# Kernel tuning notes

Hardware: AMD Instinct MI355X
Metric: run time of the kernel (lower is better)

## Reference

```python
import jax, jax.numpy as jnp
import numpy as np

B, G, C, Hmlp, R = 4, 2048, 384, 1536, 96
NH = 6          # attention heads
V = 6           # number of 2D views (len(out_transform_2d))
NC = 1024       # number of clusters for segment_csr
GX = GY = 32    # grid shape per view
SCALE_FACTOR = 0.5  # args.scale_factor
COEF_PRO = 0.5      # args.coef_pro
EPS_LN = 1e-5
EPS_BN = 1e-5


def _forward(x, center1, norm1_g, norm1_b, qkv_w, proj_w, proj_b, norm2_g, norm2_b,
             fc1_w, fc1_b, fc2_w, fc2_b, ada1_w, ada1_b, ada2_w, ada2_b,
             bn3_g, bn3_b, bn3_m, bn3_v, bn2_g, bn2_b, bn2_m, bn2_v,
             norm3_g, norm3_b, a1_qkv_w, a1_proj_w, a1_proj_b,
             mask, idx_ptr, sorted_cluster_indices, cluster, flat_grid_index,
             grid_shape_x, grid_shape_y):
    B_, G1, C_ = x.shape
    hd = C_ // NH

    def ln(t, g, b):
        mu = t.mean(-1, keepdims=True)
        var = ((t - mu) ** 2).mean(-1, keepdims=True)
        return (t - mu) * jax.lax.rsqrt(var + EPS_LN) * g + b

    def bn_gelu(t, g, b, m, v):  # BatchNorm1d (eval) + GELU
        t = (t - m) * jax.lax.rsqrt(v + EPS_BN) * g + b
        return jax.nn.gelu(t, approximate=False)

    # ---- multi-head self-attention sublayer ----
    h = ln(x, norm1_g, norm1_b)
    qkv = (h @ qkv_w).reshape(B_, G1, 3, NH, hd).transpose(2, 0, 3, 1, 4)
    q, k, v = qkv[0], qkv[1], qkv[2]
    attn = jax.nn.softmax(jnp.einsum('bhqd,bhkd->bhqk', q, k) * hd ** -0.5, axis=-1)
    o = jnp.einsum('bhqk,bhkd->bhqd', attn, v).transpose(0, 2, 1, 3).reshape(B_, G1, C_)
    x = x + o @ proj_w + proj_b

    # ---- MLP + adapter sublayer ----
    h2 = ln(x, norm2_g, norm2_b)
    ffn = jax.nn.gelu(h2 @ fc1_w + fc1_b, approximate=False) @ fc2_w + fc2_b
    a = ffn @ ada1_w + ada1_b
    a = a * jax.nn.sigmoid(1.702 * a)      # QuickGELU
    ada = a @ ada2_w + ada2_b
    x = x + ffn + SCALE_FACTOR * ada

    cls_x = x[:, :1]
    pts = x[:, 1:]
    Gp = G1 - 1
    N = B_ * Gp

    # ---- 3D branch: segment_csr max/mean over clusters, gather back ----
    feat = pts.reshape(N, C_)
    fs = feat[sorted_cluster_indices]
    seg = cluster[sorted_cluster_indices]          # sorted segment ids (CSR order)
    nc = idx_ptr.shape[0] - 1
    cnt = jax.ops.segment_sum(jnp.ones((N,), feat.dtype), seg, nc)
    fsum = jax.ops.segment_sum(fs, seg, nc)
    fmax = jax.ops.segment_max(fs, seg, nc)
    fmax = jnp.where(cnt[:, None] > 0, fmax, 0.0)
    fmean = fsum / jnp.maximum(cnt, 1.0)[:, None]
    x3d = bn_gelu(fmax + fmean, bn3_g, bn3_b, bn3_m, bn3_v)[cluster].reshape(pts.shape)

    # ---- per-view 2D branch: masked attn + scatter_max/mean over grid cells ----
    dim_size = center1.shape[0] * grid_shape_x * grid_shape_y
    nviews = center1.shape[1]
    views = []
    for i in range(nviews):
        fx = pts.reshape(N, C_)
        h3 = ln(fx, norm3_g[i], norm3_b[i]).reshape(B_, Gp, C_)
        qkv1 = (h3 @ a1_qkv_w[i]).reshape(B_, Gp, 3, C_).transpose(2, 0, 1, 3)
        q1, k1, v1 = qkv1[0], qkv1[1], qkv1[2]
        s = jnp.einsum('bqd,bkd->bqk', q1, k1) * C_ ** -0.5
        s = jnp.where(mask[i][None], s, jnp.finfo(s.dtype).min)
        o1 = jnp.einsum('bqk,bkd->bqd', jax.nn.softmax(s, axis=-1), v1) @ a1_proj_w[i] + a1_proj_b[i]
        fx = o1.reshape(N, C_) + fx
        gi = flat_grid_index[i]
        gc = jax.ops.segment_sum(jnp.ones((N,), fx.dtype), gi, dim_size)
        gs = jax.ops.segment_sum(fx, gi, dim_size)
        gm = jax.ops.segment_max(fx, gi, dim_size)
        gm = jnp.where(gc[:, None] > 0, gm, 0.0)
        cell = bn_gelu(gs / jnp.maximum(gc, 1.0)[:, None] + gm,
                       bn2_g[i], bn2_b[i], bn2_m[i], bn2_v[i])
        views.append(cell[gi].reshape(pts.shape))

    # ---- cosine-similarity weighted fusion across views ----
    x_sup = jnp.stack(views, 0)                     # [V,B,G,C]
    dot = jnp.sum(x_sup * x3d[None], -1)
    nrm = jnp.linalg.norm(x_sup, axis=-1) * jnp.linalg.norm(x3d, axis=-1)[None]
    sims = (dot / jnp.maximum(nrm, 1e-8) + 1.0) / 2.0
    sims = sims / sims.sum(0, keepdims=True)
    x_sup_w = jnp.sum(x_sup * sims[..., None], 0)
    pts = pts + COEF_PRO * x_sup_w
    return jnp.concatenate([cls_x, pts], axis=1)


def setup_inputs() -> dict:
    rng = np.random.default_rng(0)
    key = jax.random.key(0)
    N = B * G
    # consistent cluster structure: every cluster non-empty
    cluster = np.concatenate([np.arange(NC), rng.integers(0, NC, N - NC)]).astype(np.int32)
    rng.shuffle(cluster)
    sorted_idx = np.argsort(cluster, kind='stable').astype(np.int32)
    counts = np.bincount(cluster, minlength=NC)
    idx_ptr = np.concatenate([[0], np.cumsum(counts)]).astype(np.int32)
    flat_grid_index = rng.integers(0, B * GX * GY, (V, N)).astype(np.int32)
    mask = (rng.random((V, G, G)) < 0.25) | np.eye(G, dtype=bool)[None]
    ks = jax.random.split(key, 16)
    f32 = jnp.float32
    def w(k, shape, s=0.02):
        return jax.random.normal(k, shape, f32) * s
    return {
        'x': jax.random.normal(ks[0], (B, G + 1, C), f32),
        'center1': jax.random.normal(ks[1], (B, V, G, 3), f32),
        'norm1_g': jnp.ones((C,), f32), 'norm1_b': jnp.zeros((C,), f32),
        'qkv_w': w(ks[2], (C, 3 * C)), 'proj_w': w(ks[3], (C, C)), 'proj_b': jnp.zeros((C,), f32),
        'norm2_g': jnp.ones((C,), f32), 'norm2_b': jnp.zeros((C,), f32),
        'fc1_w': w(ks[4], (C, Hmlp)), 'fc1_b': jnp.zeros((Hmlp,), f32),
        'fc2_w': w(ks[5], (Hmlp, C)), 'fc2_b': jnp.zeros((C,), f32),
        'ada1_w': w(ks[6], (C, R)), 'ada1_b': jnp.zeros((R,), f32),
        'ada2_w': w(ks[7], (R, C)), 'ada2_b': jnp.zeros((C,), f32),
        'bn3_g': jnp.ones((C,), f32), 'bn3_b': jnp.zeros((C,), f32),
        'bn3_m': w(ks[8], (C,), 0.1), 'bn3_v': jnp.ones((C,), f32) + jax.random.uniform(ks[9], (C,), f32) * 0.5,
        'bn2_g': jnp.ones((V, C), f32), 'bn2_b': jnp.zeros((V, C), f32),
        'bn2_m': w(ks[10], (V, C), 0.1), 'bn2_v': jnp.ones((V, C), f32) + jax.random.uniform(ks[11], (V, C), f32) * 0.5,
        'norm3_g': jnp.ones((V, C), f32), 'norm3_b': jnp.zeros((V, C), f32),
        'a1_qkv_w': w(ks[12], (V, C, 3 * C)), 'a1_proj_w': w(ks[13], (V, C, C)), 'a1_proj_b': jnp.zeros((V, C), f32),
        'mask': jnp.asarray(mask),
        'idx_ptr': jnp.asarray(idx_ptr),
        'sorted_cluster_indices': jnp.asarray(sorted_idx),
        'cluster': jnp.asarray(cluster),
        'flat_grid_index': jnp.asarray(flat_grid_index),
        'grid_shape_x': GX,
        'grid_shape_y': GY,
    }


def reference(x, center1, norm1_g, norm1_b, qkv_w, proj_w, proj_b, norm2_g, norm2_b,
              fc1_w, fc1_b, fc2_w, fc2_b, ada1_w, ada1_b, ada2_w, ada2_b,
              bn3_g, bn3_b, bn3_m, bn3_v, bn2_g, bn2_b, bn2_m, bn2_v,
              norm3_g, norm3_b, a1_qkv_w, a1_proj_w, a1_proj_b,
              mask, idx_ptr, sorted_cluster_indices, cluster, flat_grid_index,
              grid_shape_x, grid_shape_y):
    return _forward(x, center1, norm1_g, norm1_b, qkv_w, proj_w, proj_b, norm2_g, norm2_b,
                    fc1_w, fc1_b, fc2_w, fc2_b, ada1_w, ada1_b, ada2_w, ada2_b,
                    bn3_g, bn3_b, bn3_m, bn3_v, bn2_g, bn2_b, bn2_m, bn2_v,
                    norm3_g, norm3_b, a1_qkv_w, a1_proj_w, a1_proj_b,
                    mask, idx_ptr, sorted_cluster_indices, cluster, flat_grid_index,
                    grid_shape_x, grid_shape_y)
```

## Files before the change

### kernel.cpp

```cpp
#include <hip/hip_runtime.h>
#include <math.h>

typedef short bf16x8 __attribute__((ext_vector_type(8)));
typedef float f32x4 __attribute__((ext_vector_type(4)));

#define GLL16(g, l) \
  __builtin_amdgcn_global_load_lds((__attribute__((address_space(1))) const unsigned int*)(g), \
                                   (__attribute__((address_space(3))) unsigned int*)(l), 16, 0, 0)

__device__ __forceinline__ float wsum(float v){
  #pragma unroll
  for (int o=32;o;o>>=1) v += __shfl_xor(v,o);
  return v;
}
__device__ __forceinline__ float geluf(float x){
  return 0.5f*x*(1.0f+erff(x*0.7071067811865475f));
}
__device__ __forceinline__ short fbf(float f){
  unsigned u = __float_as_uint(f);
  unsigned r = (u + 0x7fffu + ((u>>16)&1u)) >> 16;
  return (short)r;
}
__device__ __forceinline__ float bff(short s){
  return __uint_as_float(((unsigned)(unsigned short)s)<<16);
}
__device__ __forceinline__ unsigned fkey(float f){
  unsigned b=__float_as_uint(f);
  return (b&0x80000000u)? ~b : (b|0x80000000u);
}
__device__ __forceinline__ float fdec(unsigned k){
  unsigned b=(k&0x80000000u)? (k&0x7fffffffu) : ~k;
  return __uint_as_float(b);
}

__global__ void detect_mask_kernel(const int* __restrict__ m, long long n, int* flag){
  long long i = (long long)blockIdx.x*256 + threadIdx.x;
  bool bad = (i<n) && (m[i]!=0 && m[i]!=1);
  if (__any(bad)) { if ((threadIdx.x&63)==0) atomicOr(flag,1); }
}
__global__ void mask_byte_kernel(const void* __restrict__ m, unsigned char* __restrict__ mb,
                                 long long n4, const int* __restrict__ flag){
  long long i = (long long)blockIdx.x*256 + threadIdx.x;
  if (i>=n4) return;
  int mode = *flag;
  uchar4 o;
  if (mode){ o = ((const uchar4*)m)[i]; o.x=o.x!=0; o.y=o.y!=0; o.z=o.z!=0; o.w=o.w!=0; }
  else { int4 v = ((const int4*)m)[i];
         o.x=(unsigned char)(v.x!=0); o.y=(unsigned char)(v.y!=0);
         o.z=(unsigned char)(v.z!=0); o.w=(unsigned char)(v.w!=0); }
  ((uchar4*)mb)[i]=o;
}

__device__ __forceinline__ float epi(float v, const float* bias, int col, int act){
  if (bias) v += bias[col];
  if (act==1) v = geluf(v);
  else if (act==2) v = v*(1.f/(1.f+__expf(-1.702f*v)));
  return v;
}

#define XBM 128
#define XBN 128
#define XBK 32
__global__ __launch_bounds__(256)
void gemm_bf16_big(const short* __restrict__ A, int lda, long long sA,
                   const short* __restrict__ B, int ldb, long long sB,
                   const float* __restrict__ bias, long long sBias,
                   const float* __restrict__ res, int ldr, long long sR,
                   void* __restrict__ out, int ldo, long long sO, int outbf16,
                   int M, int N, int K, int act, int KS)
{
  __shared__ short As[XBM*XBK];
  __shared__ short Bs[XBN*XBK];
  int zz = blockIdx.z;
  int z = zz / KS, ks = zz - z*KS;
  A += (long long)z*sA; B += (long long)z*sB;
  if (res) res += (long long)z*sR;
  if (bias) bias += (long long)z*sBias;
  float* outF = (float*)out + (long long)z*sO;
  short* outH = (short*)out + (long long)z*sO;

  int tid = threadIdx.x;
  int rowBase = blockIdx.y*XBM;
  int colBase = blockIdx.x*XBN;

  int Kc = ((K + KS*XBK - 1)/(KS*XBK))*XBK;
  int kbeg = ks*Kc;
  int kend = min(K, kbeg+Kc);
  if (kbeg >= kend) return;

  int w = tid>>6;
  int lane = tid&63;
  int lm = lane&15, quad = lane>>4;
  int waveM = w>>1, waveN = w&1;

  int arow0 = min(rowBase + w*32 + lm,      M-1);
  int arow1 = min(rowBase + w*32 + 16 + lm, M-1);
  int brow0 = min(colBase + w*32 + lm,      N-1);
  int brow1 = min(colBase + w*32 + 16 + lm, N-1);
  const short* Ag0 = A + (long long)arow0*lda + quad*8;
  const short* Ag1 = A + (long long)arow1*lda + quad*8;
  const short* Bg0 = B + (long long)brow0*ldb + quad*8;
  const short* Bg1 = B + (long long)brow1*ldb + quad*8;
  short* Al0 = &As[(w*2+0)*512];
  short* Al1 = &As[(w*2+1)*512];
  short* Bl0 = &Bs[(w*2+0)*512];
  short* Bl1 = &Bs[(w*2+1)*512];

  f32x4 acc[4][4] = {};

  for (int k0=kbeg; k0<kend; k0+=XBK){
    GLL16(Ag0 + k0, Al0);
    GLL16(Ag1 + k0, Al1);
    GLL16(Bg0 + k0, Bl0);
    GLL16(Bg1 + k0, Bl1);
    __syncthreads();
    bf16x8 af[4], bfr[4];
    #pragma unroll
    for (int tm=0;tm<4;tm++) af[tm]  = *(bf16x8*)&As[(waveM*4+tm)*512 + quad*128 + lm*8];
    #pragma unroll
    for (int tn=0;tn<4;tn++) bfr[tn] = *(bf16x8*)&Bs[(waveN*4+tn)*512 + quad*128 + lm*8];
    #pragma unroll
    for (int tm=0;tm<4;tm++)
      #pragma unroll
      for (int tn=0;tn<4;tn++)
        acc[tm][tn] = __builtin_amdgcn_mfma_f32_16x16x32_bf16(af[tm], bfr[tn], acc[tm][tn], 0,0,0);
    __syncthreads();
  }

  #pragma unroll
  for (int tm=0;tm<4;tm++){
    #pragma unroll
    for (int tn=0;tn<4;tn++){
      int col = colBase + waveN*64 + tn*16 + lm;
      if (col>=N) continue;
      #pragma unroll
      for (int reg=0;reg<4;reg++){
        int row = rowBase + waveM*64 + tm*16 + quad*4 + reg;
        if (row>=M) continue;
        float v = acc[tm][tn][reg];
        if (KS>1){ atomicAdd(&outF[(long long)row*ldo+col], v); continue; }
        v = epi(v, bias, col, act);
        if (res) v += res[(long long)row*ldr+col];
        if (outbf16) outH[(long long)row*ldo+col] = fbf(v);
        else         outF[(long long)row*ldo+col] = v;
      }
    }
  }
}

__global__ __launch_bounds__(256)
void gemm_bf16_s(const short* __restrict__ A, int lda, long long sA,
                 const short* __restrict__ B, int ldb, long long sB,
                 const float* __restrict__ bias, long long sBias,
                 const float* __restrict__ res, int ldr, long long sR,
                 void* __restrict__ out, int ldo, long long sO, int outbf16,
                 int M, int N, int K, int act)
{
  __shared__ short As[64*32];
  __shared__ short Bs[64*32];
  int z = blockIdx.z;
  A += (long long)z*sA; B += (long long)z*sB;
  if (res) res += (long long)z*sR;
  if (bias) bias += (long long)z*sBias;
  float* outF = (float*)out + (long long)z*sO;
  short* outH = (short*)out + (long long)z*sO;

  int tid = threadIdx.x;
  int rowBase = blockIdx.y*64;
  int colBase = blockIdx.x*64;

  int w = tid>>6;
  int lane = tid&63;
  int lm = lane&15, quad = lane>>4;
  int wm = w>>1, wn = w&1;

  int arow = min(rowBase + w*16 + lm, M-1);
  int brow = min(colBase + w*16 + lm, N-1);
  const short* Ag = A + (long long)arow*lda + quad*8;
  const short* Bg = B + (long long)brow*ldb + quad*8;
  short* Al = &As[w*512];
  short* Bl = &Bs[w*512];

  f32x4 acc[2][2] = {};

  for (int k0=0; k0<K; k0+=32){
    GLL16(Ag + k0, Al);
    GLL16(Bg + k0, Bl);
    __syncthreads();
    bf16x8 af[2], bfr[2];
    #pragma unroll
    for (int tm=0;tm<2;tm++) af[tm]  = *(bf16x8*)&As[(wm*2+tm)*512 + quad*128 + lm*8];
    #pragma unroll
    for (int tn=0;tn<2;tn++) bfr[tn] = *(bf16x8*)&Bs[(wn*2+tn)*512 + quad*128 + lm*8];
    #pragma unroll
    for (int tm=0;tm<2;tm++)
      #pragma unroll
      for (int tn=0;tn<2;tn++)
        acc[tm][tn] = __builtin_amdgcn_mfma_f32_16x16x32_bf16(af[tm], bfr[tn], acc[tm][tn], 0,0,0);
    __syncthreads();
  }

  #pragma unroll
  for (int tm=0;tm<2;tm++){
    #pragma unroll
    for (int tn=0;tn<2;tn++){
      int col = colBase + wn*32 + tn*16 + lm;
      if (col>=N) continue;
      #pragma unroll
      for (int reg=0;reg<4;reg++){
        int row = rowBase + wm*32 + tm*16 + quad*4 + reg;
        if (row>=M) continue;
        float v = epi(acc[tm][tn][reg], bias, col, act);
        if (res) v += res[(long long)row*ldr+col];
        if (outbf16==2){
          int bb = row>>11;
          outH[((long long)bb*384 + col)*2048 + (row&2047)] = fbf(v);
        }
        else if (outbf16) outH[(long long)row*ldo+col] = fbf(v);
        else              outF[(long long)row*ldo+col] = v;
      }
    }
  }
}

__global__ __launch_bounds__(256,2)
void flash_view(const short* __restrict__ QK6, const short* __restrict__ Vt6,
                const unsigned char* __restrict__ maskb, short* __restrict__ O6)
{
  __shared__ char lds[58112];
  const float scale = 0.05103103630798288f;
  int id = blockIdx.x;
  int xcd = id & 7;
  int j = id >> 3;
  int vb = xcd*3 + (j>>5);
  int qt = j & 31;
  int v = vb >> 2, b = vb & 3;
  int tid=threadIdx.x, w=tid>>6, lane=tid&63, lm=lane&15, quad=lane>>4;

  const short* Qp = QK6 + ((long long)v*8192 + b*2048 + qt*64)*768;
  const short* Kp = QK6 + ((long long)v*8192 + b*2048)*768 + 384;
  const short* Vp = Vt6 + (long long)(v*4+b)*384*2048;
  const unsigned char* Mp = maskb + (long long)v*2048*2048 + (long long)qt*64*2048;
  short* Op = O6 + ((long long)v*8192 + b*2048 + qt*64)*384;

  short* P = (short*)(lds + 49152);
  float* alphaL = (float*)(lds + 57856);

  bf16x8 af[12];
  #pragma unroll
  for (int c=0;c<12;c++)
    af[c] = *(const bf16x8*)(Qp + (long long)(w*16+lm)*768 + c*32 + quad*8);

  float m_i[4], l_i[4];
  #pragma unroll
  for (int r=0;r<4;r++){ m_i[r]=-3.0e38f; l_i[r]=0.f; }
  f32x4 Oacc[4][6] = {};

  #pragma unroll
  for (int c=0;c<12;c++)
    GLL16(Kp + (long long)(w*16 + lm)*768 + c*32 + quad*8, (short*)(lds + w*12288 + c*1024));

  for (int kt=0; kt<32; kt++){
    __syncthreads();
    unsigned char mreg[4][4];
    #pragma unroll
    for (int ct=0;ct<4;ct++)
      #pragma unroll
      for (int r=0;r<4;r++)
        mreg[ct][r] = Mp[(long long)(w*16+quad*4+r)*2048 + kt*64 + ct*16 + lm];
    f32x4 S[4];
    #pragma unroll
    for (int i=0;i<4;i++) S[i] = (f32x4){0.f,0.f,0.f,0.f};
    #pragma unroll
    for (int kc=0;kc<12;kc++){
      #pragma unroll
      for (int ct=0;ct<4;ct++){
        bf16x8 bf = *(bf16x8*)(lds + ct*12288 + kc*1024 + quad*256 + lm*16);
        S[ct] = __builtin_amdgcn_mfma_f32_16x16x32_bf16(af[kc], bf, S[ct], 0,0,0);
      }
    }
    #pragma unroll
    for (int ct=0;ct<4;ct++){
      #pragma unroll
      for (int r=0;r<4;r++)
        S[ct][r] = mreg[ct][r] ? S[ct][r]*scale : -3.0e38f;
    }
    float alpha[4], mnew[4];
    #pragma unroll
    for (int r=0;r<4;r++){
      float rm = S[0][r];
      #pragma unroll
      for (int ct=1;ct<4;ct++) rm = fmaxf(rm, S[ct][r]);
      #pragma unroll
      for (int o=1;o<16;o<<=1) rm = fmaxf(rm, __shfl_xor(rm, o));
      mnew[r] = fmaxf(m_i[r], rm);
      alpha[r] = __expf(m_i[r]-mnew[r]);
      m_i[r] = mnew[r];
    }
    float rs[4] = {0.f,0.f,0.f,0.f};
    #pragma unroll
    for (int ct=0;ct<4;ct++){
      #pragma unroll
      for (int r=0;r<4;r++){
        float sv = S[ct][r];
        float p = (sv > -1.0e37f) ? __expf(sv - mnew[r]) : 0.f;
        rs[r] += p;
        P[(w*16+quad*4+r)*68 + ct*16 + lm] = fbf(p);
      }
    }
    #pragma unroll
    for (int r=0;r<4;r++){
      #pragma unroll
      for (int o=1;o<16;o<<=1) rs[r] += __shfl_xor(rs[r], o);
      l_i[r] = l_i[r]*alpha[r] + rs[r];
    }
    if (lm==0){
      #pragma unroll
      for (int r=0;r<4;r++) alphaL[w*16+quad*4+r] = alpha[r];
    }
    bf16x8 Vreg[6][2];
    #pragma unroll
    for (int jj=0;jj<6;jj++)
      #pragma unroll
      for (int kk=0;kk<2;kk++)
        Vreg[jj][kk] = *(const bf16x8*)(Vp + (long long)((w*6+jj)*16+lm)*2048 + kt*64 + kk*32 + quad*8);
    __syncthreads();
    if (kt < 31){
      #pragma unroll
      for (int c=0;c<12;c++)
        GLL16(Kp + (long long)((kt+1)*64 + w*16 + lm)*768 + c*32 + quad*8,
              (short*)(lds + w*12288 + c*1024));
    }
    f32x4 am[4];
    #pragma unroll
    for (int m=0;m<4;m++) am[m] = *(f32x4*)&alphaL[m*16 + quad*4];
    #pragma unroll
    for (int m=0;m<4;m++)
      #pragma unroll
      for (int tn=0;tn<6;tn++)
        Oacc[m][tn] *= am[m];
    #pragma unroll
    for (int kk=0;kk<2;kk++){
      bf16x8 ap[4];
      #pragma unroll
      for (int m=0;m<4;m++) ap[m] = *(bf16x8*)&P[(m*16+lm)*68 + kk*32 + quad*8];
      #pragma unroll
      for (int tn=0;tn<6;tn++){
        #pragma unroll
        for (int m=0;m<4;m++)
          Oacc[m][tn] = __builtin_amdgcn_mfma_f32_16x16x32_bf16(ap[m], Vreg[tn][kk], Oacc[m][tn], 0,0,0);
      }
    }
  }

  __syncthreads();
  if (lm==0){
    #pragma unroll
    for (int r=0;r<4;r++) alphaL[w*16+quad*4+r] = l_i[r];
  }
  __syncthreads();
  f32x4 lv[4];
  #pragma unroll
  for (int m=0;m<4;m++) lv[m] = *(f32x4*)&alphaL[m*16 + quad*4];
  #pragma unroll
  for (int m=0;m<4;m++){
    #pragma unroll
    for (int tn=0;tn<6;tn++){
      #pragma unroll
      for (int reg=0;reg<4;reg++){
        Op[(long long)(m*16+quad*4+reg)*384 + (w*6+tn)*16 + lm] = fbf(Oacc[m][tn][reg] / lv[m][reg]);
      }
    }
  }
}

__global__ __launch_bounds__(256,4)
void flash_inner(const short* __restrict__ QKV, const short* __restrict__ Vt,
                 short* __restrict__ O)
{
  __shared__ char lds[17152];
  int id = blockIdx.x;
  int xcd = id & 7;
  int j = id >> 3;
  int bh = xcd*3 + j/33;
  int qt = j%33;
  int b=bh/6, h=bh-b*6;
  int tid=threadIdx.x, w=tid>>6, lane=tid&63, lm=lane&15, quad=lane>>4;

  const short* Qb = QKV + (long long)b*2049*1152 + h*64;
  const short* Kb = Qb + 384;
  const short* Vtp = Vt + (long long)bh*64*2112;
  short* Op = O + ((long long)b*2049 + qt*64)*384 + h*64;

  short* P = (short*)(lds + 8192);
  float* alphaL = (float*)(lds + 16896);

  int qr = min(qt*64 + w*16 + lm, 2048);
  bf16x8 af[2];
  #pragma unroll
  for (int c=0;c<2;c++)
    af[c] = *(const bf16x8*)(Qb + (long long)qr*1152 + c*32 + quad*8);

  float m_i[4], l_i[4];
  #pragma unroll
  for (int r=0;r<4;r++){ m_i[r]=-3.0e38f; l_i[r]=0.f; }
  f32x4 Oacc[4] = {};

  {
    int kr0 = min(w*16 + lm, 2048);
    #pragma unroll
    for (int c=0;c<2;c++)
      GLL16(Kb + (long long)kr0*1152 + c*32 + quad*8, (short*)(lds + w*2048 + c*1024));
  }

  for (int kt=0; kt<33; kt++){
    __syncthreads();
    f32x4 S[4];
    #pragma unroll
    for (int i=0;i<4;i++) S[i] = (f32x4){0.f,0.f,0.f,0.f};
    #pragma unroll
    for (int kc=0;kc<2;kc++){
      #pragma unroll
      for (int ct=0;ct<4;ct++){
        bf16x8 bf = *(bf16x8*)(lds + ct*2048 + kc*1024 + quad*256 + lm*16);
        S[ct] = __builtin_amdgcn_mfma_f32_16x16x32_bf16(af[kc], bf, S[ct], 0,0,0);
      }
    }
    #pragma unroll
    for (int ct=0;ct<4;ct++){
      int scol = kt*64 + ct*16 + lm;
      bool ok = scol <= 2048;
      #pragma unroll
      for (int r=0;r<4;r++) S[ct][r] = ok ? S[ct][r]*0.125f : -3.0e38f;
    }
    float alpha[4], mnew[4];
    #pragma unroll
    for (int r=0;r<4;r++){
      float rm = S[0][r];
      #pragma unroll
      for (int ct=1;ct<4;ct++) rm = fmaxf(rm, S[ct][r]);
      #pragma unroll
      for (int o=1;o<16;o<<=1) rm = fmaxf(rm, __shfl_xor(rm, o));
      mnew[r] = fmaxf(m_i[r], rm);
      alpha[r] = __expf(m_i[r]-mnew[r]);
      m_i[r] = mnew[r];
    }
    float rs[4] = {0.f,0.f,0.f,0.f};
    #pragma unroll
    for (int ct=0;ct<4;ct++){
      #pragma unroll
      for (int r=0;r<4;r++){
        float sv = S[ct][r];
        float p = (sv > -1.0e37f) ? __expf(sv - mnew[r]) : 0.f;
        rs[r] += p;
        P[(w*16+quad*4+r)*68 + ct*16 + lm] = fbf(p);
      }
    }
    #pragma unroll
    for (int r=0;r<4;r++){
      #pragma unroll
      for (int o=1;o<16;o<<=1) rs[r] += __shfl_xor(rs[r], o);
      l_i[r] = l_i[r]*alpha[r] + rs[r];
    }
    if (lm==0){
      #pragma unroll
      for (int r=0;r<4;r++) alphaL[w*16+quad*4+r] = alpha[r];
    }
    bf16x8 Vreg[2];
    #pragma unroll
    for (int kk=0;kk<2;kk++)
      Vreg[kk] = *(const bf16x8*)(Vtp + (long long)(w*16+lm)*2112 + kt*64 + kk*32 + quad*8);
    __syncthreads();
    if (kt < 32){
      int krn = min((kt+1)*64 + w*16 + lm, 2048);
      #pragma unroll
      for (int c=0;c<2;c++)
        GLL16(Kb + (long long)krn*1152 + c*32 + quad*8, (short*)(lds + w*2048 + c*1024));
    }
    f32x4 am[4];
    #pragma unroll
    for (int m=0;m<4;m++) am[m] = *(f32x4*)&alphaL[m*16 + quad*4];
    #pragma unroll
    for (int m=0;m<4;m++) Oacc[m] *= am[m];
    #pragma unroll
    for (int kk=0;kk<2;kk++){
      bf16x8 ap[4];
      #pragma unroll
      for (int m=0;m<4;m++) ap[m] = *(bf16x8*)&P[(m*16+lm)*68 + kk*32 + quad*8];
      #pragma unroll
      for (int m=0;m<4;m++)
        Oacc[m] = __builtin_amdgcn_mfma_f32_16x16x32_bf16(ap[m], Vreg[kk], Oacc[m], 0,0,0);
    }
  }

  __syncthreads();
  if (lm==0){
    #pragma unroll
    for (int r=0;r<4;r++) alphaL[w*16+quad*4+r] = l_i[r];
  }
  __syncthreads();
  f32x4 lv[4];
  #pragma unroll
  for (int m=0;m<4;m++) lv[m] = *(f32x4*)&alphaL[m*16 + quad*4];
  #pragma unroll
  for (int m=0;m<4;m++){
    #pragma unroll
    for (int reg=0;reg<4;reg++){
      int row = qt*64 + m*16 + quad*4 + reg;
      if (row < 2049)
        Op[(long long)(m*16+quad*4+reg)*384 + w*16 + lm] = fbf(Oacc[m][reg] / lv[m][reg]);
    }
  }
}

__global__ __launch_bounds__(128)
void ln_bf16_kernel(const float* __restrict__ in, const float* __restrict__ g,
                    const float* __restrict__ bt, short* __restrict__ out)
{
  long long row = blockIdx.x;
  const float* p = in + row*384;
  int tid = threadIdx.x;
  float v0=p[tid], v1=p[tid+128], v2=p[tid+256];
  float s = v0+v1+v2;
  float ss = v0*v0+v1*v1+v2*v2;
  __shared__ float r1[2], r2[2];
  s = wsum(s); ss = wsum(ss);
  int wid=tid>>6, lane=tid&63;
  if (lane==0){ r1[wid]=s; r2[wid]=ss; }
  __syncthreads();
  float mean=(r1[0]+r1[1])*(1.f/384.f);
  float var =(r2[0]+r2[1])*(1.f/384.f)-mean*mean;
  float rstd=rsqrtf(var+1e-5f);
  short* o = out + row*384;
  o[tid]     = fbf((v0-mean)*rstd*g[tid]+bt[tid]);
  o[tid+128] = fbf((v1-mean)*rstd*g[tid+128]+bt[tid+128]);
  o[tid+256] = fbf((v2-mean)*rstd*g[tid+256]+bt[tid+256]);
}

__global__ __launch_bounds__(128)
void ln6_kernel(const float* __restrict__ in, const float* __restrict__ g6,
                const float* __restrict__ b6, short* __restrict__ out6)
{
  long long row = blockIdx.x;
  const float* p = in + row*384;
  int tid = threadIdx.x;
  float v0=p[tid], v1=p[tid+128], v2=p[tid+256];
  float s = v0+v1+v2;
  float ss = v0*v0+v1*v1+v2*v2;
  __shared__ float r1[2], r2[2];
  s = wsum(s); ss = wsum(ss);
  int wid=tid>>6, lane=tid&63;
  if (lane==0){ r1[wid]=s; r2[wid]=ss; }
  __syncthreads();
  float mean=(r1[0]+r1[1])*(1.f/384.f);
  float var =(r2[0]+r2[1])*(1.f/384.f)-mean*mean;
  float rstd=rsqrtf(var+1e-5f);
  float n0=(v0-mean)*rstd, n1=(v1-mean)*rstd, n2=(v2-mean)*rstd;
  #pragma unroll
  for (int i=0;i<6;i++){
    const float* g = g6 + i*384;
    const float* bt = b6 + i*384;
    short* o = out6 + (long long)i*8192*384 + row*384;
    o[tid]     = fbf(n0*g[tid]+bt[tid]);
    o[tid+128] = fbf(n1*g[tid+128]+bt[tid+128]);
    o[tid+256] = fbf(n2*g[tid+256]+bt[tid+256]);
  }
}

__global__ void cvt_kernel(const float* __restrict__ in, short* __restrict__ out, long long n4){
  long long i = (long long)blockIdx.x*256 + threadIdx.x;
  if (i<n4){
    float4 f = ((const float4*)in)[i];
    short4 s;
    s.x=fbf(f.x); s.y=fbf(f.y); s.z=fbf(f.z); s.w=fbf(f.w);
    ((short4*)out)[i]=s;
  }
}

__global__ __launch_bounds__(256)
void tconv_kernel(const float* __restrict__ in, int ldin, long long sIn, long long sIn2, int zmod,
                  int R, int C, short* __restrict__ out, int ldout, long long sOut)
{
  __shared__ float tile[32][33];
  int z = blockIdx.z;
  const float* ip = in + (long long)(z/zmod)*sIn + (long long)(z%zmod)*sIn2;
  short* op = out + (long long)z*sOut;
  int r0 = blockIdx.x*32;
  int c0 = blockIdx.y*32;
  int tx = threadIdx.x&31, ty = threadIdx.x>>5;
  #pragma unroll
  for (int i=0;i<4;i++){
    int r = r0 + ty + i*8, c = c0 + tx;
    tile[ty+i*8][tx] = (r<R && c<C) ? ip[(long long)r*ldin + c] : 0.f;
  }
  __syncthreads();
  #pragma unroll
  for (int i=0;i<4;i++){
    int oc = c0 + ty + i*8;
    int orr = r0 + tx;
    if (oc<C && orr<ldout) op[(long long)oc*ldout + orr] = fbf(tile[tx][ty+i*8]);
  }
}

__global__ __launch_bounds__(256)
void tconv16_kernel(const short* __restrict__ in, int ldin, long long sIn, long long sIn2, int zmod,
                    int R, int C, short* __restrict__ out, int ldout, long long sOut)
{
  __shared__ short tile[32][34];
  int z = blockIdx.z;
  const short* ip = in + (long long)(z/zmod)*sIn + (long long)(z%zmod)*sIn2;
  short* op = out + (long long)z*sOut;
  int r0 = blockIdx.x*32;
  int c0 = blockIdx.y*32;
  int tx = threadIdx.x&31, ty = threadIdx.x>>5;
  #pragma unroll
  for (int i=0;i<4;i++){
    int r = r0 + ty + i*8, c = c0 + tx;
    tile[ty+i*8][tx] = (r<R && c<C) ? ip[(long long)r*ldin + c] : (short)0;
  }
  __syncthreads();
  #pragma unroll
  for (int i=0;i<4;i++){
    int oc = c0 + ty + i*8;
    int orr = r0 + tx;
    if (oc<C && orr<ldout) op[(long long)oc*ldout + orr] = tile[tx][ty+i*8];
  }
}

__global__ void ew_x2_kernel(float* x1, const float* ffn, const float* ada, long long n){
  long long i=(long long)blockIdx.x*256+threadIdx.x;
  if (i<n) x1[i] = x1[i] + ffn[i] + 0.5f*ada[i];
}
__global__ void copy_pts_kernel(const float* __restrict__ x2, float* __restrict__ pts){
  long long i=(long long)blockIdx.x*256+threadIdx.x;
  if (i < 8192ll*384){
    long long b = i/(2048ll*384);
    long long rem = i%(2048ll*384);
    pts[i] = x2[(b*2049+1)*384 + rem];
  }
}
__global__ void copy_cls_kernel(const float* __restrict__ x2, float* __restrict__ out){
  int i = blockIdx.x*256+threadIdx.x;
  if (i < 4*384){
    int b=i/384, c=i%384;
    out[(long long)b*2049*384 + c] = x2[(long long)b*2049*384 + c];
  }
}

__global__ __launch_bounds__(128)
void scatter_seg_kernel(const float* __restrict__ feat, const int* __restrict__ seg,
                        float* __restrict__ fsum, unsigned* __restrict__ fmax,
                        float* __restrict__ cnt,
                        long long zFeat, long long zSeg, long long zSum, long long zCnt)
{
  int n = blockIdx.x, z = blockIdx.y;
  feat += (long long)z*zFeat; seg += (long long)z*zSeg;
  fsum += (long long)z*zSum; fmax += (long long)z*zSum; cnt += (long long)z*zCnt;
  int s = seg[n];
  const float* p = feat + (long long)n*384;
  int tid = threadIdx.x;
  #pragma unroll
  for (int k=0;k<3;k++){
    int c = tid + k*128;
    float v = p[c];
    atomicAdd(&fsum[(long long)s*384+c], v);
    atomicMax(&fmax[(long long)s*384+c], fkey(v));
  }
  if (tid==0) atomicAdd(&cnt[s], 1.0f);
}

__global__ __launch_bounds__(128)
void cell_kernel(const float* __restrict__ fsum, const unsigned* __restrict__ fmax,
                 const float* __restrict__ cnt,
                 const float* __restrict__ g, const float* __restrict__ bb,
                 const float* __restrict__ m, const float* __restrict__ v,
                 float* __restrict__ out, long long zSum, long long zCnt, long long zP)
{
  int s = blockIdx.x, z = blockIdx.y;
  fsum += (long long)z*zSum; fmax += (long long)z*zSum; cnt += (long long)z*zCnt;
  g += (long long)z*zP; bb += (long long)z*zP; m += (long long)z*zP; v += (long long)z*zP;
  out += (long long)z*zSum;
  float cn = cnt[s];
  float denom = fmaxf(cn, 1.f);
  int tid = threadIdx.x;
  #pragma unroll
  for (int k=0;k<3;k++){
    int c = tid + k*128;
    float mx = (cn>0.f) ? fdec(fmax[(long long)s*384+c]) : 0.f;
    float t = mx + fsum[(long long)s*384+c]/denom;
    t = (t - m[c])*rsqrtf(v[c]+1e-5f)*g[c] + bb[c];
    out[(long long)s*384+c] = geluf(t);
  }
}

__global__ __launch_bounds__(128)
void combine_kernel(const float* __restrict__ pts, const float* __restrict__ cell3,
                    const int* __restrict__ cluster, const float* __restrict__ cell2,
                    const int* __restrict__ gidx, float* __restrict__ out)
{
  int n = blockIdx.x;
  int tid = threadIdx.x;
  __shared__ float sdot[6], ssq[6], sw[6];
  __shared__ int soff[6];
  __shared__ float red[2][2];
  __shared__ float sn3;
  const float* x3 = cell3 + (long long)cluster[n]*384;
  int wid=tid>>6, lane=tid&63;
  float sq=0.f;
  for (int c=tid;c<384;c+=128){ float v=x3[c]; sq+=v*v; }
  sq = wsum(sq);
  if (lane==0) red[0][wid]=sq;
  __syncthreads();
  if (tid==0) sn3 = sqrtf(red[0][0]+red[0][1]);
  __syncthreads();
  for (int i=0;i<6;i++){
    int gi = gidx[(long long)i*8192 + n];
    if (tid==0) soff[i]=gi;
    const float* r = cell2 + ((long long)i*4096 + gi)*384;
    float d=0.f, s2=0.f;
    for (int c=tid;c<384;c+=128){ float a=r[c]; d+=a*x3[c]; s2+=a*a; }
    d = wsum(d); s2 = wsum(s2);
    if (lane==0){ red[0][wid]=d; red[1][wid]=s2; }
    __syncthreads();
    if (tid==0){ sdot[i]=red[0][0]+red[0][1]; ssq[i]=red[1][0]+red[1][1]; }
    __syncthreads();
  }
  if (tid==0){
    float ssumv=0.f; float sims[6];
    for (int i=0;i<6;i++){
      float nrm = sqrtf(ssq[i])*sn3;
      float s = (sdot[i]/fmaxf(nrm,1e-8f) + 1.f)*0.5f;
      sims[i]=s; ssumv+=s;
    }
    for (int i=0;i<6;i++) sw[i]=sims[i]/ssumv;
  }
  __syncthreads();
  int b = n>>11, gp = n&2047;
  float* o = out + ((long long)(b*2049 + 1 + gp))*384;
  for (int c=tid;c<384;c+=128){
    float acc=0.f;
    #pragma unroll
    for (int i=0;i<6;i++){
      const float* r = cell2 + ((long long)i*4096 + soff[i])*384;
      acc += sw[i]*r[c];
    }
    o[c] = pts[(long long)n*384+c] + 0.5f*acc;
  }
}

static inline void launch_gemm16b(hipStream_t s, const short* A,int lda,long long sA,
  const short* B,int ldb,long long sB, const float* bias, long long sBias,
  const float* res,int ldr,long long sR, void* out,int ldo,long long sO,int outbf16,
  int M,int N,int K,int act,int nz,int KS)
{
  dim3 g((N+XBN-1)/XBN,(M+XBM-1)/XBM,(unsigned)(nz*KS));
  hipLaunchKernelGGL(gemm_bf16_big,g,dim3(256),0,s,
    A,lda,sA,B,ldb,sB,bias,sBias,res,ldr,sR,out,ldo,sO,outbf16,M,N,K,act,KS);
}
static inline void launch_gemm16s(hipStream_t s, const short* A,int lda,long long sA,
  const short* B,int ldb,long long sB, const float* bias, long long sBias,
  const float* res,int ldr,long long sR, void* out,int ldo,long long sO,int outbf16,
  int M,int N,int K,int act,int nz)
{
  dim3 g((N+63)/64,(M+63)/64,(unsigned)nz);
  hipLaunchKernelGGL(gemm_bf16_s,g,dim3(256),0,s,
    A,lda,sA,B,ldb,sB,bias,sBias,res,ldr,sR,out,ldo,sO,outbf16,M,N,K,act);
}
static inline void launch_tconv(hipStream_t s, const float* in,int ldin,long long sIn,long long sIn2,int zmod,
  int R,int C, short* out,int ldout,long long sOut,int nz)
{
  dim3 g((ldout+31)/32,(C+31)/32,(unsigned)nz);
  hipLaunchKernelGGL(tconv_kernel,g,dim3(256),0,s, in,ldin,sIn,sIn2,zmod,R,C,out,ldout,sOut);
}
static inline void launch_tconv16(hipStream_t s, const short* in,int ldin,long long sIn,long long sIn2,int zmod,
  int R,int C, short* out,int ldout,long long sOut,int nz)
{
  dim3 g((ldout+31)/32,(C+31)/32,(unsigned)nz);
  hipLaunchKernelGGL(tconv16_kernel,g,dim3(256),0,s, in,ldin,sIn,sIn2,zmod,R,C,out,ldout,sOut);
}
static inline void launch_cvt(hipStream_t s, const float* in, short* out, long long n){
  long long n4 = n/4;
  hipLaunchKernelGGL(cvt_kernel,dim3((unsigned)((n4+255)/256)),dim3(256),0,s,in,out,n4);
}

extern "C" void kernel_launch(void* const* d_in, const int* in_sizes, int n_in,
                              void* d_out, int out_size, void* d_ws, size_t ws_size,
                              hipStream_t stream)
{
  const float* x       = (const float*)d_in[0];
  const float* norm1_g = (const float*)d_in[2];
  const float* norm1_b = (const float*)d_in[3];
  const float* qkv_w   = (const float*)d_in[4];
  const float* proj_w  = (const float*)d_in[5];
  const float* proj_b  = (const float*)d_in[6];
  const float* norm2_g = (const float*)d_in[7];
  const float* norm2_b = (const float*)d_in[8];
  const float* fc1_w   = (const float*)d_in[9];
  const float* fc1_b   = (const float*)d_in[10];
  const float* fc2_w   = (const float*)d_in[11];
  const float* fc2_b   = (const float*)d_in[12];
  const float* ada1_w  = (const float*)d_in[13];
  const float* ada1_b  = (const float*)d_in[14];
  const float* ada2_w  = (const float*)d_in[15];
  const float* ada2_b  = (const float*)d_in[16];
  const float* bn3_g   = (const float*)d_in[17];
  const float* bn3_b   = (const float*)d_in[18];
  const float* bn3_m   = (const float*)d_in[19];
  const float* bn3_v   = (const float*)d_in[20];
  const float* bn2_g   = (const float*)d_in[21];
  const float* bn2_b   = (const float*)d_in[22];
  const float* bn2_m   = (const float*)d_in[23];
  const float* bn2_v   = (const float*)d_in[24];
  const float* norm3_g = (const float*)d_in[25];
  const float* norm3_b = (const float*)d_in[26];
  const float* a1_qkv_w  = (const float*)d_in[27];
  const float* a1_proj_w = (const float*)d_in[28];
  const float* a1_proj_b = (const float*)d_in[29];
  const void*  maskp     = d_in[30];
  const int*   cluster   = (const int*)d_in[33];
  const int*   fgi       = (const int*)d_in[34];
  float* out = (float*)d_out;

  size_t off = 0;
  char* wsb = (char*)d_ws;
  auto alloc = [&](size_t bytes)->void*{
    void* p = wsb + off;
    off += (bytes + 255) & ~(size_t)255;
    return p;
  };
  short*    bufHh = (short*)alloc(8196ll*384*2);
  float*    ptsb  = (float*)alloc(8192ll*384*4);
  float*    cnt   = (float*)alloc(1024*4);
  float*    fsum  = (float*)alloc(1024ll*384*4);
  unsigned* fmaxe = (unsigned*)alloc(1024ll*384*4);
  float*    cell3 = (float*)alloc(1024ll*384*4);
  unsigned char* maskb = (unsigned char*)alloc(6ll*2048*2048);
  float*    gc6   = (float*)alloc(6ll*4096*4);
  short*    qkvT  = (short*)alloc(1152ll*384*2);
  short*    projT = (short*)alloc(384ll*384*2);
  short*    fc1T  = (short*)alloc(1536ll*384*2);
  short*    fc2T  = (short*)alloc(384ll*1536*2);
  short*    ada1T = (short*)alloc(96ll*384*2);
  short*    ada2T = (short*)alloc(384ll*96*2);
  short*    a1qkvT  = (short*)alloc(6ll*1152*384*2);
  short*    a1projT = (short*)alloc(6ll*384*384*2);
  int*      flag  = (int*)alloc(256);
  char* arena = (char*)alloc(188743680);
  char* A0 = arena;
  char* A1 = arena + 75497472;
  char* A2 = arena + 150994944;
  short* bufQh = (short*)(A0 + 0);
  float* bufO  = (float*)(A0 + 20971520);
  short* bufOh = (short*)(A0 + 35651584);
  short* bufAh = (short*)(A0 + 44040192);
  float* bufX  = (float*)(A0 + 46137344);
  float* bufAda= (float*)(A0 + 0);
  short* Vt_i  = (short*)(A1 + 0);
  short* bufTh = (short*)(A1 + 8388608);
  short* QK6   = (short*)(A0 + 0);
  short* Vt6   = (short*)(A1 + 0);
  short* O6    = (short*)(A2 + 0);
  short* bufHh6= (short*)(A2 + 0);
  float* bufT6 = (float*)(A0 + 0);
  float* gsum6 = (float*)(A1 + 0);
  unsigned* gmaxe6 = (unsigned*)(A1 + 37748736);
  float* cell2 = (float*)(A0 + 0);

  hipMemsetAsync(flag, 0, 4, stream);
  {
    long long nInt = 6ll*2048*2048/4;
    detect_mask_kernel<<<dim3((unsigned)((nInt+255)/256)),dim3(256),0,stream>>>((const int*)maskp, nInt, flag);
    mask_byte_kernel<<<dim3((unsigned)((nInt+255)/256)),dim3(256),0,stream>>>(maskp, maskb, nInt, flag);
  }

  launch_tconv(stream, qkv_w, 1152, 0,0,1, 384,1152, qkvT, 384, 0, 1);
  launch_tconv(stream, proj_w, 384, 0,0,1, 384,384,  projT, 384, 0, 1);
  launch_tconv(stream, fc1_w, 1536, 0,0,1, 384,1536, fc1T, 384, 0, 1);
  launch_tconv(stream, fc2_w, 384,  0,0,1, 1536,384, fc2T, 1536, 0, 1);
  launch_tconv(stream, ada1_w, 96,  0,0,1, 384,96,   ada1T, 384, 0, 1);
  launch_tconv(stream, ada2_w, 384, 0,0,1, 96,384,   ada2T, 96, 0, 1);
  launch_tconv(stream, a1_qkv_w, 1152, 384ll*1152,0,1, 384,1152, a1qkvT, 384, 1152ll*384, 6);
  launch_tconv(stream, a1_proj_w, 384, 384ll*384,0,1, 384,384,  a1projT, 384, 384ll*384, 6);

  ln_bf16_kernel<<<8196,128,0,stream>>>(x, norm1_g, norm1_b, bufHh);
  launch_gemm16b(stream, bufHh,384,0, qkvT,384,0, nullptr,0, nullptr,0,0,
                 bufQh,1152,0,1, 8196,1152,384, 0, 1,1);
  launch_tconv16(stream, bufQh + 768, 1152, 2049ll*1152, 64, 6, 2049, 64, Vt_i, 2112, 64ll*2112, 24);
  flash_inner<<<dim3(792),256,0,stream>>>(bufQh, Vt_i, bufOh);
  launch_gemm16s(stream, bufOh,384,0, projT,384,0, proj_b,0, x,384,0,
                 bufX,384,0,0, 8196,384,384, 0, 1);
  ln_bf16_kernel<<<8196,128,0,stream>>>(bufX, norm2_g, norm2_b, bufHh);
  launch_gemm16b(stream, bufHh,384,0, fc1T,384,0, fc1_b,0, nullptr,0,0,
                 bufTh,1536,0,1, 8196,1536,384, 1, 1,1);
  launch_gemm16s(stream, bufTh,1536,0, fc2T,1536,0, fc2_b,0, nullptr,0,0,
                 bufO,384,0,0, 8196,384,1536, 0, 1);
  launch_cvt(stream, bufO, bufOh, 8196ll*384);
  launch_gemm16s(stream, bufOh,384,0, ada1T,384,0, ada1_b,0, nullptr,0,0,
                 bufAh,96,0,1, 8196,96,384, 2, 1);
  launch_gemm16s(stream, bufAh,96,0, ada2T,96,0, ada2_b,0, nullptr,0,0,
                 bufAda,384,0,0, 8196,384,96, 0, 1);
  ew_x2_kernel<<<dim3((8196*384+255)/256),256,0,stream>>>(bufX, bufO, bufAda, 8196ll*384);
  copy_cls_kernel<<<6,256,0,stream>>>(bufX, out);
  copy_pts_kernel<<<dim3((8192*384+255)/256),256,0,stream>>>(bufX, ptsb);

  hipMemsetAsync(cnt, 0, 1024*4, stream);
  hipMemsetAsync(fsum, 0, 1024ll*384*4, stream);
  hipMemsetAsync(fmaxe, 0, 1024ll*384*4, stream);
  scatter_seg_kernel<<<dim3(8192,1),128,0,stream>>>(ptsb, cluster, fsum, fmaxe, cnt, 0,0,0,0);
  cell_kernel<<<dim3(1024,1),128,0,stream>>>(fsum, fmaxe, cnt, bn3_g,bn3_b,bn3_m,bn3_v, cell3, 0,0,0);

  ln6_kernel<<<8192,128,0,stream>>>(ptsb, norm3_g, norm3_b, bufHh6);
  launch_gemm16b(stream, bufHh6,384,8192ll*384, a1qkvT,384,1152ll*384,
                 nullptr,0, nullptr,0,0, QK6,768,8192ll*768,1, 8192,768,384, 0, 6,1);
  launch_gemm16s(stream, bufHh6,384,8192ll*384, a1qkvT + 768ll*384,384,1152ll*384,
                 nullptr,0, nullptr,0,0, Vt6,2048,4ll*384*2048,2, 8192,384,384, 0, 6);

  flash_view<<<dim3(768),256,0,stream>>>(QK6, Vt6, maskb, O6);

  launch_gemm16s(stream, O6,384,8192ll*384, a1projT,384,384ll*384,
                 a1_proj_b,384, ptsb,384,0,
                 bufT6,384,8192ll*384,0, 8192,384,384, 0, 6);
  hipMemsetAsync(gc6, 0, 6ll*4096*4, stream);
  hipMemsetAsync(gsum6, 0, 6ll*4096*384*4, stream);
  hipMemsetAsync(gmaxe6, 0, 6ll*4096*384*4, stream);
  scatter_seg_kernel<<<dim3(8192,6),128,0,stream>>>(bufT6, fgi, gsum6, gmaxe6, gc6,
      8192ll*384, 8192, 4096ll*384, 4096);
  cell_kernel<<<dim3(4096,6),128,0,stream>>>(gsum6, gmaxe6, gc6,
      bn2_g, bn2_b, bn2_m, bn2_v, cell2, 4096ll*384, 4096, 384);

  combine_kernel<<<8192,128,0,stream>>>(ptsb, cell3, cluster, cell2, fgi, out);
}
```

Measured before the change: 1.596 ms.

## Bit-pack attention mask, reschedule K loads, and raise MFMA wave priority

Replaces the byte-per-element mask with a 64-bit bitmask per row chunk, so each flash_view thread loads four 64-bit words instead of sixteen scattered bytes per tile. The K-tile global-to-LDS load moves from after the second barrier (prefetching the next tile) to the top of each iteration. s_setprio is raised around the MFMA blocks in both flash kernels. Removing the prefetch loses overlap of the K load with the PV MFMAs, which could offset the smaller mask traffic.

```diff
diff --git a/kernel.cpp b/kernel.cpp
--- a/kernel.cpp
+++ b/kernel.cpp
@@ -38,17 +38,33 @@
   bool bad = (i<n) && (m[i]!=0 && m[i]!=1);
   if (__any(bad)) { if ((threadIdx.x&63)==0) atomicOr(flag,1); }
 }
-__global__ void mask_byte_kernel(const void* __restrict__ m, unsigned char* __restrict__ mb,
-                                 long long n4, const int* __restrict__ flag){
+__global__ void mask_bits_kernel(const void* __restrict__ m, unsigned long long* __restrict__ mb,
+                                 long long nOut, const int* __restrict__ flag){
   long long i = (long long)blockIdx.x*256 + threadIdx.x;
-  if (i>=n4) return;
+  if (i>=nOut) return;
   int mode = *flag;
-  uchar4 o;
-  if (mode){ o = ((const uchar4*)m)[i]; o.x=o.x!=0; o.y=o.y!=0; o.z=o.z!=0; o.w=o.w!=0; }
-  else { int4 v = ((const int4*)m)[i];
-         o.x=(unsigned char)(v.x!=0); o.y=(unsigned char)(v.y!=0);
-         o.z=(unsigned char)(v.z!=0); o.w=(unsigned char)(v.w!=0); }
-  ((uchar4*)mb)[i]=o;
+  unsigned long long bits = 0;
+  if (mode){
+    const unsigned long long* p = (const unsigned long long*)((const unsigned char*)m + i*64);
+    #pragma unroll
+    for (int k=0;k<8;k++){
+      unsigned long long v = p[k];
+      #pragma unroll
+      for (int b=0;b<8;b++)
+        bits |= (unsigned long long)(((v>>(b*8))&0xffull)!=0) << (k*8+b);
+    }
+  } else {
+    const int4* p = (const int4*)((const int*)m + i*64);
+    #pragma unroll
+    for (int k=0;k<16;k++){
+      int4 v = p[k];
+      bits |= (unsigned long long)(v.x!=0) << (k*4+0);
+      bits |= (unsigned long long)(v.y!=0) << (k*4+1);
+      bits |= (unsigned long long)(v.z!=0) << (k*4+2);
+      bits |= (unsigned long long)(v.w!=0) << (k*4+3);
+    }
+  }
+  mb[i] = bits;
 }
 
 __device__ __forceinline__ float epi(float v, const float* bias, int col, int act){
@@ -225,7 +241,7 @@
 
 __global__ __launch_bounds__(256,2)
 void flash_view(const short* __restrict__ QK6, const short* __restrict__ Vt6,
-                const unsigned char* __restrict__ maskb, short* __restrict__ O6)
+                const unsigned long long* __restrict__ maskbits, short* __restrict__ O6)
 {
   __shared__ char lds[58112];
   const float scale = 0.05103103630798288f;
@@ -240,7 +256,7 @@
   const short* Qp = QK6 + ((long long)v*8192 + b*2048 + qt*64)*768;
   const short* Kp = QK6 + ((long long)v*8192 + b*2048)*768 + 384;
   const short* Vp = Vt6 + (long long)(v*4+b)*384*2048;
-  const unsigned char* Mp = maskb + (long long)v*2048*2048 + (long long)qt*64*2048;
+  const unsigned long long* Mb = maskbits + (long long)v*2048*32 + (long long)qt*64*32;
   short* Op = O6 + ((long long)v*8192 + b*2048 + qt*64)*384;
 
   short* P = (short*)(lds + 49152);
@@ -256,21 +272,19 @@
   for (int r=0;r<4;r++){ m_i[r]=-3.0e38f; l_i[r]=0.f; }
   f32x4 Oacc[4][6] = {};
 
-  #pragma unroll
-  for (int c=0;c<12;c++)
-    GLL16(Kp + (long long)(w*16 + lm)*768 + c*32 + quad*8, (short*)(lds + w*12288 + c*1024));
-
   for (int kt=0; kt<32; kt++){
+    #pragma unroll
+    for (int c=0;c<12;c++)
+      GLL16(Kp + (long long)(kt*64 + w*16 + lm)*768 + c*32 + quad*8, (short*)(lds + w*12288 + c*1024));
     __syncthreads();
-    unsigned char mreg[4][4];
-    #pragma unroll
-    for (int ct=0;ct<4;ct++)
-      #pragma unroll
-      for (int r=0;r<4;r++)
-        mreg[ct][r] = Mp[(long long)(w*16+quad*4+r)*2048 + kt*64 + ct*16 + lm];
+    unsigned long long mb[4];
+    #pragma unroll
+    for (int r=0;r<4;r++)
+      mb[r] = Mb[(long long)(w*16+quad*4+r)*32 + kt];
     f32x4 S[4];
     #pragma unroll
     for (int i=0;i<4;i++) S[i] = (f32x4){0.f,0.f,0.f,0.f};
+    __builtin_amdgcn_s_setprio(1);
     #pragma unroll
     for (int kc=0;kc<12;kc++){
       #pragma unroll
@@ -279,11 +293,14 @@
         S[ct] = __builtin_amdgcn_mfma_f32_16x16x32_bf16(af[kc], bf, S[ct], 0,0,0);
       }
     }
-    #pragma unroll
-    for (int ct=0;ct<4;ct++){
-      #pragma unroll
-      for (int r=0;r<4;r++)
-        S[ct][r] = mreg[ct][r] ? S[ct][r]*scale : -3.0e38f;
+    __builtin_amdgcn_s_setprio(0);
+    #pragma unroll
+    for (int r=0;r<4;r++){
+      unsigned long long t = mb[r] >> lm;
+      S[0][r] = ((unsigned)t      & 1u) ? S[0][r]*scale : -3.0e38f;
+      S[1][r] = ((unsigned)(t>>16)& 1u) ? S[1][r]*scale : -3.0e38f;
+      S[2][r] = ((unsigned)(t>>32)& 1u) ? S[2][r]*scale : -3.0e38f;
+      S[3][r] = ((unsigned)(t>>48)& 1u) ? S[3][r]*scale : -3.0e38f;
     }
     float alpha[4], mnew[4];
     #pragma unroll
@@ -325,12 +342,6 @@
       for (int kk=0;kk<2;kk++)
         Vreg[jj][kk] = *(const bf16x8*)(Vp + (long long)((w*6+jj)*16+lm)*2048 + kt*64 + kk*32 + quad*8);
     __syncthreads();
-    if (kt < 31){
-      #pragma unroll
-      for (int c=0;c<12;c++)
-        GLL16(Kp + (long long)((kt+1)*64 + w*16 + lm)*768 + c*32 + quad*8,
-              (short*)(lds + w*12288 + c*1024));
-    }
     f32x4 am[4];
     #pragma unroll
     for (int m=0;m<4;m++) am[m] = *(f32x4*)&alphaL[m*16 + quad*4];
@@ -339,6 +350,7 @@
       #pragma unroll
       for (int tn=0;tn<6;tn++)
         Oacc[m][tn] *= am[m];
+    __builtin_amdgcn_s_setprio(1);
     #pragma unroll
     for (int kk=0;kk<2;kk++){
       bf16x8 ap[4];
@@ -351,6 +363,7 @@
           Oacc[m][tn] = __builtin_amdgcn_mfma_f32_16x16x32_bf16(ap[m], Vreg[tn][kk], Oacc[m][tn], 0,0,0);
       }
     }
+    __builtin_amdgcn_s_setprio(0);
   }
 
   __syncthreads();
@@ -418,6 +431,7 @@
     f32x4 S[4];
     #pragma unroll
     for (int i=0;i<4;i++) S[i] = (f32x4){0.f,0.f,0.f,0.f};
+    __builtin_amdgcn_s_setprio(1);
     #pragma unroll
     for (int kc=0;kc<2;kc++){
       #pragma unroll
@@ -426,6 +440,7 @@
         S[ct] = __builtin_amdgcn_mfma_f32_16x16x32_bf16(af[kc], bf, S[ct], 0,0,0);
       }
     }
+    __builtin_amdgcn_s_setprio(0);
     #pragma unroll
     for (int ct=0;ct<4;ct++){
       int scol = kt*64 + ct*16 + lm;
@@ -482,6 +497,7 @@
     for (int m=0;m<4;m++) am[m] = *(f32x4*)&alphaL[m*16 + quad*4];
     #pragma unroll
     for (int m=0;m<4;m++) Oacc[m] *= am[m];
+    __builtin_amdgcn_s_setprio(1);
     #pragma unroll
     for (int kk=0;kk<2;kk++){
       bf16x8 ap[4];
@@ -491,6 +507,7 @@
       for (int m=0;m<4;m++)
         Oacc[m] = __builtin_amdgcn_mfma_f32_16x16x32_bf16(ap[m], Vreg[kk], Oacc[m], 0,0,0);
     }
+    __builtin_amdgcn_s_setprio(0);
   }
 
   __syncthreads();
@@ -866,11 +883,14 @@
   unsigned* gmaxe6 = (unsigned*)(A1 + 37748736);
   float* cell2 = (float*)(A0 + 0);
 
+  unsigned long long* maskbits = (unsigned long long*)maskb;
+
   hipMemsetAsync(flag, 0, 4, stream);
   {
     long long nInt = 6ll*2048*2048/4;
     detect_mask_kernel<<<dim3((unsigned)((nInt+255)/256)),dim3(256),0,stream>>>((const int*)maskp, nInt, flag);
-    mask_byte_kernel<<<dim3((unsigned)((nInt+255)/256)),dim3(256),0,stream>>>(maskp, maskb, nInt, flag);
+    long long nOut = 6ll*2048*32;
+    mask_bits_kernel<<<dim3((unsigned)((nOut+255)/256)),dim3(256),0,stream>>>(maskp, maskbits, nOut, flag);
   }
 
   launch_tconv(stream, qkv_w, 1152, 0,0,1, 384,1152, qkvT, 384, 0, 1);
@@ -915,7 +935,7 @@
   launch_gemm16s(stream, bufHh6,384,8192ll*384, a1qkvT + 768ll*384,384,1152ll*384,
                  nullptr,0, nullptr,0,0, Vt6,2048,4ll*384*2048,2, 8192,384,384, 0, 6);
 
-  flash_view<<<dim3(768),256,0,stream>>>(QK6, Vt6, maskb, O6);
+  flash_view<<<dim3(768),256,0,stream>>>(QK6, Vt6, maskbits, O6);
 
   launch_gemm16s(stream, O6,384,8192ll*384, a1projT,384,384ll*384,
                  a1_proj_b,384, ptsb,384,0,
```

Result: faster. 1.546 ms (-3.2%).
